# Kernel tuning notes

Measured on AMD Instinct MI355X. Metric: run time of the kernel, lower is better.

## Reference

```python
import jax, jax.numpy as jnp
import numpy as np

B, S, D, H, F = 2, 4096, 768, 12, 3072
DK = D // H
EPS = 1e-5


def _layernorm(x, alpha, gamma):
    # Faithful to the custom Layernormalization: torch.std (unbiased, ddof=1),
    # (x - mean) / (std + eps), scalar alpha/gamma.
    m = jnp.mean(x, axis=-1, keepdims=True)
    s = jnp.std(x, axis=-1, ddof=1, keepdims=True)
    return alpha * ((x - m) / (s + EPS)) + gamma


def setup_inputs() -> dict:
    key = jax.random.key(0)
    ks = jax.random.split(key, 12)
    sc = 0.02
    inp = {
        "x": jax.random.normal(ks[0], (B, S, D), jnp.float32),
        # attention projections, stored as [in, out]
        "wq": jax.random.normal(ks[1], (D, D), jnp.float32) * sc,
        "bq": jnp.zeros((D,), jnp.float32),
        "wk": jax.random.normal(ks[2], (D, D), jnp.float32) * sc,
        "bk": jnp.zeros((D,), jnp.float32),
        "wv": jax.random.normal(ks[3], (D, D), jnp.float32) * sc,
        "bv": jnp.zeros((D,), jnp.float32),
        "wo": jax.random.normal(ks[4], (D, D), jnp.float32) * sc,
        "bo": jnp.zeros((D,), jnp.float32),
        # feedforward
        "w1": jax.random.normal(ks[5], (D, F), jnp.float32) * sc,
        "b1": jnp.zeros((F,), jnp.float32),
        "w2": jax.random.normal(ks[6], (F, D), jnp.float32) * sc,
        "b2": jnp.zeros((D,), jnp.float32),
        # two residual LayerNorms, scalar params (alpha=1, gamma=0 at init)
        "a1": jnp.ones((1,), jnp.float32),
        "g1": jnp.zeros((1,), jnp.float32),
        "a2": jnp.ones((1,), jnp.float32),
        "g2": jnp.zeros((1,), jnp.float32),
    }
    return inp


def reference(x, wq, bq, wk, bk, wv, bv, wo, bo, w1, b1, w2, b2, a1, g1, a2, g2):
    # --- self attention sublayer ---
    q = (x @ wq + bq).reshape(B, S, H, DK).transpose(0, 2, 1, 3)  # [B,H,S,dk]
    k = (x @ wk + bk).reshape(B, S, H, DK).transpose(0, 2, 1, 3)
    v = (x @ wv + bv).reshape(B, S, H, DK).transpose(0, 2, 1, 3)
    scores = jnp.einsum("bhqd,bhkd->bhqk", q, k) / np.sqrt(DK).astype(np.float32)
    attn = jax.nn.softmax(scores, axis=-1)  # dropout is identity (p=0 / eval)
    ctx = jnp.einsum("bhqk,bhkd->bhqd", attn, v)  # [B,H,S,dk]
    ctx = ctx.transpose(0, 2, 1, 3).reshape(B, S, D)
    attn_out = ctx @ wo + bo
    x = _layernorm(x + attn_out, a1, g1)
    # --- feedforward sublayer ---
    ff = jax.nn.relu(x @ w1 + b1) @ w2 + b2
    x = _layernorm(x + ff, a2, g2)
    return x
```

## Files before the change

kernel.cpp:

```cpp
#include <hip/hip_runtime.h>
#include <hip/hip_bf16.h>
#include <cstdint>
#include <cstddef>

typedef unsigned short u16;
typedef __attribute__((ext_vector_type(8))) __bf16 bf16x8;
typedef __attribute__((ext_vector_type(4))) float f32x4;

#define AS1 __attribute__((address_space(1)))
#define AS3 __attribute__((address_space(3)))

__device__ __forceinline__ u16 f2bf(float f) {
    union { float f; uint32_t u; } v; v.f = f;
    uint32_t r = (v.u + 0x7FFFu + ((v.u >> 16) & 1u)) >> 16;
    return (u16)r;
}

__device__ __forceinline__ float bf2f(u16 b) {
    union { uint32_t u; float f; } v; v.u = ((uint32_t)b) << 16;
    return v.f;
}

__device__ __forceinline__ uint32_t pack_bf2(float lo, float hi) {
    __hip_bfloat162 p = __float22bfloat162_rn(float2{lo, hi});
    union { __hip_bfloat162 b; uint32_t u; } v; v.b = p;
    return v.u;
}

__device__ __forceinline__ f32x4 mfma16(bf16x8 a, bf16x8 b, f32x4 c) {
    return __builtin_amdgcn_mfma_f32_16x16x32_bf16(a, b, c, 0, 0, 0);
}

__device__ __forceinline__ void async16(const u16* g, u16* lds_uniform_base) {
    __builtin_amdgcn_global_load_lds((const AS1 void*)g, (AS3 void*)lds_uniform_base, 16, 0, 0);
}

__global__ __launch_bounds__(256)
void k_prep(const float* __restrict__ x, u16* __restrict__ xb,
            const float* __restrict__ wq, const float* __restrict__ wk,
            const float* __restrict__ wv, const float* __restrict__ wo,
            const float* __restrict__ w1, const float* __restrict__ w2,
            u16* __restrict__ wqkvt, u16* __restrict__ wot,
            u16* __restrict__ w1t, u16* __restrict__ w2t)
{
    int bx = blockIdx.x;
    if (bx < 6144) {
        int i = (bx * 256 + threadIdx.x) * 4;
        float4 f = *(const float4*)(x + i);
        xb[i + 0] = f2bf(f.x); xb[i + 1] = f2bf(f.y);
        xb[i + 2] = f2bf(f.z); xb[i + 3] = f2bf(f.w);
        return;
    }
    int t = bx - 6144;
    const float* in; u16* out; int R, C;
    if (t < 2304) {
        int m = t / 576; t -= m * 576;
        R = 768; C = 768;
        in = (m == 0) ? wq : (m == 1) ? wk : (m == 2) ? wv : wo;
        out = (m < 3) ? wqkvt + (size_t)m * 768 * 768 : wot;
    } else if (t < 4608) {
        t -= 2304; in = w1; out = w1t; R = 768; C = 3072;
    } else {
        t -= 4608; in = w2; out = w2t; R = 3072; C = 768;
    }
    int tilesX = C >> 5;
    int c0 = (t % tilesX) * 32, r0 = (t / tilesX) * 32;
    __shared__ float tile[32][33];
    int tx = threadIdx.x & 31, ty = threadIdx.x >> 5;
    #pragma unroll
    for (int i = ty; i < 32; i += 8)
        tile[i][tx] = in[(size_t)(r0 + i) * C + c0 + tx];
    __syncthreads();
    #pragma unroll
    for (int i = ty; i < 32; i += 8)
        out[(size_t)(c0 + i) * R + r0 + tx] = f2bf(tile[tx][i]);
}

template <bool RELU>
__global__ __launch_bounds__(256)
void k_gemm(const u16* __restrict__ A, const u16* __restrict__ Bt,
            const float* __restrict__ bias, u16* __restrict__ Cb,
            int M, int N, int K)
{
    __shared__ __align__(16) u16 lA[128 * 32];
    __shared__ __align__(16) u16 lB[128 * 32];
    const int tid = threadIdx.x;
    const int w = tid >> 6, lane = tid & 63;
    const int quad = lane >> 4, l15 = lane & 15;
    const int m0 = blockIdx.x * 128, n0 = blockIdx.y * 128;
    const int wm = (w >> 1) * 64, wn = (w & 1) * 64;
    const int sw = (quad ^ ((l15 >> 1) & 3)) * 8;

    const f32x4 fz = {0.f, 0.f, 0.f, 0.f};
    f32x4 acc[4][4];
    #pragma unroll
    for (int i = 0; i < 4; ++i)
        #pragma unroll
        for (int j = 0; j < 4; ++j) acc[i][j] = fz;

    for (int k0 = 0; k0 < K; k0 += 32) {
        #pragma unroll
        for (int r = 0; r < 2; ++r) {
            int c = r * 256 + tid;
            int row = c >> 2, ch = (c & 3) ^ ((row >> 1) & 3);
            async16(A + (size_t)(m0 + row) * K + k0 + ch * 8,
                    (u16*)lA + (size_t)(r * 256 + w * 64) * 8);
            async16(Bt + (size_t)(n0 + row) * K + k0 + ch * 8,
                    (u16*)lB + (size_t)(r * 256 + w * 64) * 8);
        }
        __syncthreads();
        bf16x8 af[4], bfr[4];
        #pragma unroll
        for (int i = 0; i < 4; ++i)
            af[i] = *(const bf16x8*)&lA[(wm + i * 16 + l15) * 32 + sw];
        #pragma unroll
        for (int j = 0; j < 4; ++j)
            bfr[j] = *(const bf16x8*)&lB[(wn + j * 16 + l15) * 32 + sw];
        #pragma unroll
        for (int i = 0; i < 4; ++i)
            #pragma unroll
            for (int j = 0; j < 4; ++j)
                acc[i][j] = mfma16(af[i], bfr[j], acc[i][j]);
        __syncthreads();
    }
    #pragma unroll
    for (int j = 0; j < 4; ++j) {
        int col = n0 + wn + j * 16 + l15;
        float bv = bias[col];
        #pragma unroll
        for (int i = 0; i < 4; ++i) {
            int row = m0 + wm + i * 16 + quad * 4;
            #pragma unroll
            for (int r = 0; r < 4; ++r) {
                float t = acc[i][j][r] + bv;
                if (RELU) t = fmaxf(t, 0.f);
                Cb[(size_t)(row + r) * N + col] = f2bf(t);
            }
        }
    }
}

__global__ __launch_bounds__(256)
void k_gemm_part(const u16* __restrict__ A, const u16* __restrict__ Bt,
                 float* __restrict__ C0, float* __restrict__ C1,
                 int M, int N, int K, int Kh)
{
    __shared__ __align__(16) u16 lA[128 * 32];
    __shared__ __align__(16) u16 lB[128 * 32];
    const int tid = threadIdx.x;
    const int w = tid >> 6, lane = tid & 63;
    const int quad = lane >> 4, l15 = lane & 15;
    const int m0 = blockIdx.x * 128, n0 = blockIdx.y * 128;
    const int wm = (w >> 1) * 64, wn = (w & 1) * 64;
    const int sw = (quad ^ ((l15 >> 1) & 3)) * 8;
    const int kbeg = blockIdx.z * Kh, kend = kbeg + Kh;
    float* __restrict__ C = blockIdx.z ? C1 : C0;

    const f32x4 fz = {0.f, 0.f, 0.f, 0.f};
    f32x4 acc[4][4];
    #pragma unroll
    for (int i = 0; i < 4; ++i)
        #pragma unroll
        for (int j = 0; j < 4; ++j) acc[i][j] = fz;

    for (int k0 = kbeg; k0 < kend; k0 += 32) {
        #pragma unroll
        for (int r = 0; r < 2; ++r) {
            int c = r * 256 + tid;
            int row = c >> 2, ch = (c & 3) ^ ((row >> 1) & 3);
            async16(A + (size_t)(m0 + row) * K + k0 + ch * 8,
                    (u16*)lA + (size_t)(r * 256 + w * 64) * 8);
            async16(Bt + (size_t)(n0 + row) * K + k0 + ch * 8,
                    (u16*)lB + (size_t)(r * 256 + w * 64) * 8);
        }
        __syncthreads();
        bf16x8 af[4], bfr[4];
        #pragma unroll
        for (int i = 0; i < 4; ++i)
            af[i] = *(const bf16x8*)&lA[(wm + i * 16 + l15) * 32 + sw];
        #pragma unroll
        for (int j = 0; j < 4; ++j)
            bfr[j] = *(const bf16x8*)&lB[(wn + j * 16 + l15) * 32 + sw];
        #pragma unroll
        for (int i = 0; i < 4; ++i)
            #pragma unroll
            for (int j = 0; j < 4; ++j)
                acc[i][j] = mfma16(af[i], bfr[j], acc[i][j]);
        __syncthreads();
    }
    #pragma unroll
    for (int j = 0; j < 4; ++j) {
        int col = n0 + wn + j * 16 + l15;
        #pragma unroll
        for (int i = 0; i < 4; ++i) {
            int row = m0 + wm + i * 16 + quad * 4;
            #pragma unroll
            for (int r = 0; r < 4; ++r)
                C[(size_t)(row + r) * N + col] = acc[i][j][r];
        }
    }
}

__global__ __launch_bounds__(256)
void k_gemm_qkv(const u16* __restrict__ A, const u16* __restrict__ Bt,
                const float* __restrict__ bq, const float* __restrict__ bk,
                const float* __restrict__ bv,
                u16* __restrict__ qb, u16* __restrict__ kb, u16* __restrict__ vtg,
                int M, int K, float scale_q)
{
    __shared__ __align__(16) u16 qsm[4 * 64 * 72];
    u16* lA = qsm;
    u16* lB = qsm + 4096;
    const int tid = threadIdx.x;
    const int w = tid >> 6, lane = tid & 63;
    const int quad = lane >> 4, l15 = lane & 15;
    const int m0 = blockIdx.x * 128, n0 = blockIdx.y * 128;
    const int wm = (w >> 1) * 64, wn = (w & 1) * 64;
    const int sw = (quad ^ ((l15 >> 1) & 3)) * 8;
    const int sel = blockIdx.y / 6;
    const int cl0 = n0 - sel * 768;

    const f32x4 fz = {0.f, 0.f, 0.f, 0.f};
    f32x4 acc[4][4];
    #pragma unroll
    for (int i = 0; i < 4; ++i)
        #pragma unroll
        for (int j = 0; j < 4; ++j) acc[i][j] = fz;

    for (int k0 = 0; k0 < K; k0 += 32) {
        #pragma unroll
        for (int r = 0; r < 2; ++r) {
            int c = r * 256 + tid;
            int row = c >> 2, ch = (c & 3) ^ ((row >> 1) & 3);
            async16(A + (size_t)(m0 + row) * K + k0 + ch * 8,
                    lA + (size_t)(r * 256 + w * 64) * 8);
            async16(Bt + (size_t)(n0 + row) * K + k0 + ch * 8,
                    lB + (size_t)(r * 256 + w * 64) * 8);
        }
        __syncthreads();
        bf16x8 af[4], bfr[4];
        #pragma unroll
        for (int i = 0; i < 4; ++i)
            af[i] = *(const bf16x8*)&lA[(wm + i * 16 + l15) * 32 + sw];
        #pragma unroll
        for (int j = 0; j < 4; ++j)
            bfr[j] = *(const bf16x8*)&lB[(wn + j * 16 + l15) * 32 + sw];
        #pragma unroll
        for (int i = 0; i < 4; ++i)
            #pragma unroll
            for (int j = 0; j < 4; ++j)
                acc[i][j] = mfma16(af[i], bfr[j], acc[i][j]);
        __syncthreads();
    }
    const float* bias = (sel == 0) ? bq : (sel == 1) ? bk : bv;
    if (sel < 2) {
        u16* out = (sel == 0) ? qb : kb;
        float sc = (sel == 0) ? scale_q : 1.f;
        #pragma unroll
        for (int j = 0; j < 4; ++j) {
            int cl = cl0 + wn + j * 16 + l15;
            float bvv = bias[cl];
            #pragma unroll
            for (int i = 0; i < 4; ++i) {
                int row = m0 + wm + i * 16 + quad * 4;
                #pragma unroll
                for (int r = 0; r < 4; ++r)
                    out[(size_t)(row + r) * 768 + cl] = f2bf((acc[i][j][r] + bvv) * sc);
            }
        }
    } else {
        u16* lT = qsm + w * 4608;
        #pragma unroll
        for (int j = 0; j < 4; ++j) {
            float bvv = bias[cl0 + wn + j * 16 + l15];
            #pragma unroll
            for (int i = 0; i < 4; ++i)
                #pragma unroll
                for (int r = 0; r < 4; ++r)
                    lT[(j * 16 + l15) * 72 + i * 16 + quad * 4 + r]
                        = f2bf(acc[i][j][r] + bvv);
        }
        int gcol = cl0 + wn + lane;
        u16* gdst = vtg + (size_t)gcol * M + m0 + wm;
        #pragma unroll
        for (int kk = 0; kk < 8; ++kk) {
            bf16x8 v = *(const bf16x8*)&lT[lane * 72 + kk * 8];
            *(bf16x8*)(gdst + kk * 8) = v;
        }
    }
}

__global__ __launch_bounds__(256, 3)
void k_attention(const u16* __restrict__ Q, const u16* __restrict__ Kb,
                 const u16* __restrict__ Vt, u16* __restrict__ ctx,
                 int S, int D, int H, int M)
{
    __shared__ __align__(16) u16 sKV[16384];
    __shared__ float sL[2][64];
    const int qt = blockIdx.x, bh = blockIdx.y;
    const int b = bh / H, h = bh % H;
    const int tid = threadIdx.x, w = tid >> 6, lane = tid & 63;
    const int wq = w & 1, wk = w >> 1;
    const int quad = lane >> 4, l15 = lane & 15;
    const int sw = (quad ^ ((l15 >> 1) & 3)) * 8;
    const size_t bS = (size_t)b * S;
    const int q0 = qt * 128 + wq * 64;

    bf16x8 qf[4][2];
    #pragma unroll
    for (int set = 0; set < 4; ++set)
        #pragma unroll
        for (int kc = 0; kc < 2; ++kc)
            qf[set][kc] = *(const bf16x8*)(Q + (bS + q0 + set * 16 + l15) * D
                                           + (size_t)h * 64 + kc * 32 + quad * 8);

    const f32x4 fz = {0.f, 0.f, 0.f, 0.f};
    f32x4 O[4][4], Ol[4];
    #pragma unroll
    for (int s = 0; s < 4; ++s) {
        Ol[s] = fz;
        #pragma unroll
        for (int j = 0; j < 4; ++j) O[s][j] = fz;
    }
    union { u16 s[8]; bf16x8 v; } one8;
    #pragma unroll
    for (int i = 0; i < 8; ++i) one8.s[i] = 0x3F80;

    const u16* kbase = Kb + bS * D + (size_t)h * 64;
    const u16* vbase = Vt + (size_t)h * 64 * M + bS;

    const int rsw = (lane & ~12) | ((lane & 4) << 1) | ((lane & 8) >> 1);
    const u16* gk[2]; const u16* gv[2];
    #pragma unroll
    for (int i = 0; i < 2; ++i) {
        gk[i] = kbase + (size_t)rsw * D + i * 32 + w * 8;
        int c = i * 256 + tid;
        int dk = (c >> 2) & 63, vch = (c & 3) ^ ((dk >> 1) & 3);
        gv[i] = vbase + (size_t)dk * M + i * 32 + vch * 8;
    }
    const int dslot = w * 512;

    #pragma unroll
    for (int i = 0; i < 2; ++i) {
        async16(gk[i], sKV + i * 2048 + dslot);
        async16(gv[i], sKV + 8192 + i * 2048 + dslot);
        gk[i] += (size_t)64 * D;
        gv[i] += 64;
    }

    int ksl[2];
    #pragma unroll
    for (int ks = 0; ks < 2; ++ks) {
        int row64 = wk * 32 + ((l15 >> 2) << 3) + ks * 4 + (l15 & 3);
        int s = (row64 & ~12) | ((row64 & 4) << 1) | ((row64 & 8) >> 1);
        ksl[ks] = quad * 512 + s * 8;
    }

    const int T = S >> 6;
    for (int t = 0; t < T; ++t) {
        __syncthreads();
        if (t + 1 < T) {
            int nb = (t + 1) & 1;
            #pragma unroll
            for (int i = 0; i < 2; ++i) {
                async16(gk[i], sKV + nb * 4096 + i * 2048 + dslot);
                async16(gv[i], sKV + 8192 + nb * 4096 + i * 2048 + dslot);
                gk[i] += (size_t)64 * D;
                gv[i] += 64;
            }
        }
        const u16* lKb = sKV + (t & 1) * 4096;
        const u16* lVb = sKV + 8192 + (t & 1) * 4096;

        bf16x8 ka[2][2], vf[4];
        #pragma unroll
        for (int ks = 0; ks < 2; ++ks)
            #pragma unroll
            for (int kc = 0; kc < 2; ++kc)
                ka[ks][kc] = *(const bf16x8*)&lKb[kc * 2048 + ksl[ks]];
        #pragma unroll
        for (int dj = 0; dj < 4; ++dj)
            vf[dj] = *(const bf16x8*)
                &lVb[wk * 2048 + (dj * 16 + l15) * 32 + sw];

        #pragma unroll
        for (int set = 0; set < 4; ++set) {
            f32x4 sc0 = fz, sc1 = fz;
            __builtin_amdgcn_s_setprio(1);
            sc0 = mfma16(ka[0][0], qf[set][0], sc0);
            sc0 = mfma16(ka[0][1], qf[set][1], sc0);
            sc1 = mfma16(ka[1][0], qf[set][0], sc1);
            sc1 = mfma16(ka[1][1], qf[set][1], sc1);
            __builtin_amdgcn_s_setprio(0);
            float p0[4], p1[4];
            #pragma unroll
            for (int r = 0; r < 4; ++r) {
                p0[r] = __builtin_amdgcn_exp2f(sc0[r]);
                p1[r] = __builtin_amdgcn_exp2f(sc1[r]);
            }
            union { uint32_t u[4]; bf16x8 v; } pa;
            pa.u[0] = pack_bf2(p0[0], p0[1]); pa.u[1] = pack_bf2(p0[2], p0[3]);
            pa.u[2] = pack_bf2(p1[0], p1[1]); pa.u[3] = pack_bf2(p1[2], p1[3]);
            __builtin_amdgcn_s_setprio(1);
            #pragma unroll
            for (int dj = 0; dj < 4; ++dj)
                O[set][dj] = mfma16(pa.v, vf[dj], O[set][dj]);
            Ol[set] = mfma16(pa.v, one8.v, Ol[set]);
            __builtin_amdgcn_s_setprio(0);
        }
    }

    __syncthreads();
    u16* lO = sKV;
    if (wk == 1) {
        #pragma unroll
        for (int set = 0; set < 4; ++set) {
            #pragma unroll
            for (int dj = 0; dj < 4; ++dj)
                #pragma unroll
                for (int r = 0; r < 4; ++r)
                    lO[(wq * 64 + set * 16 + quad * 4 + r) * 66 + dj * 16 + l15]
                        = f2bf(O[set][dj][r]);
            if (l15 == 0) {
                #pragma unroll
                for (int r = 0; r < 4; ++r)
                    sL[wq][set * 16 + quad * 4 + r] = Ol[set][r];
            }
        }
    }
    __syncthreads();
    if (wk == 0) {
        #pragma unroll
        for (int set = 0; set < 4; ++set) {
            float rl[4];
            #pragma unroll
            for (int r = 0; r < 4; ++r)
                rl[r] = 1.f / (Ol[set][r] + sL[wq][set * 16 + quad * 4 + r]);
            #pragma unroll
            for (int dj = 0; dj < 4; ++dj)
                #pragma unroll
                for (int r = 0; r < 4; ++r) {
                    float o = O[set][dj][r]
                        + bf2f(lO[(wq * 64 + set * 16 + quad * 4 + r) * 66 + dj * 16 + l15]);
                    ctx[(bS + q0 + set * 16 + quad * 4 + r) * D
                        + (size_t)h * 64 + dj * 16 + l15] = f2bf(o * rl[r]);
                }
        }
    }
}

__global__ __launch_bounds__(256)
void k_layernorm2(const float* __restrict__ p0, const float* __restrict__ p1,
                  const float* __restrict__ resid, const float* __restrict__ bias,
                  const float* __restrict__ a, const float* __restrict__ g,
                  float* __restrict__ outf, u16* __restrict__ outb, int D)
{
    const int row = blockIdx.x, tid = threadIdx.x;
    const size_t base = (size_t)row * D;
    float v[3];
    float s = 0.f, sq = 0.f;
    #pragma unroll
    for (int i = 0; i < 3; ++i) {
        int c = tid + i * 256;
        float x = p0[base + c] + p1[base + c] + resid[base + c] + bias[c];
        v[i] = x; s += x; sq += x * x;
    }
    #pragma unroll
    for (int off = 32; off >= 1; off >>= 1) {
        s += __shfl_xor(s, off, 64);
        sq += __shfl_xor(sq, off, 64);
    }
    __shared__ float red[8];
    const int w = tid >> 6;
    if ((tid & 63) == 0) { red[w] = s; red[4 + w] = sq; }
    __syncthreads();
    s = red[0] + red[1] + red[2] + red[3];
    sq = red[4] + red[5] + red[6] + red[7];
    float mean = s / D;
    float var = fmaxf((sq - s * mean) / (D - 1), 0.f);
    float denom = sqrtf(var) + 1e-5f;
    float av = a[0], gv = g[0];
    #pragma unroll
    for (int i = 0; i < 3; ++i) {
        float y = av * ((v[i] - mean) / denom) + gv;
        if (outf) outf[base + tid + i * 256] = y;
        if (outb) outb[base + tid + i * 256] = f2bf(y);
    }
}

extern "C" void kernel_launch(void* const* d_in, const int* in_sizes, int n_in,
                              void* d_out, int out_size, void* d_ws, size_t ws_size,
                              hipStream_t stream)
{
    constexpr int B = 2, S = 4096, D = 768, H = 12, F = 3072;
    constexpr int M = B * S;
    const float SCALE_Q = 1.4426950408889634f / 8.0f;
    const float* x  = (const float*)d_in[0];
    const float* wq = (const float*)d_in[1];
    const float* bq = (const float*)d_in[2];
    const float* wk = (const float*)d_in[3];
    const float* bk = (const float*)d_in[4];
    const float* wv = (const float*)d_in[5];
    const float* bv = (const float*)d_in[6];
    const float* wo = (const float*)d_in[7];
    const float* bo = (const float*)d_in[8];
    const float* w1 = (const float*)d_in[9];
    const float* b1 = (const float*)d_in[10];
    const float* w2 = (const float*)d_in[11];
    const float* b2 = (const float*)d_in[12];
    const float* a1 = (const float*)d_in[13];
    const float* g1 = (const float*)d_in[14];
    const float* a2 = (const float*)d_in[15];
    const float* g2 = (const float*)d_in[16];

    char* ws = (char*)d_ws;
    size_t off = 0;
    auto alloc = [&](size_t bytes) {
        void* p = ws + off;
        off = (off + bytes + 255) & ~(size_t)255;
        return p;
    };
    u16*   xb    = (u16*)alloc((size_t)M * D * 2);
    u16*   wqkvt = (u16*)alloc((size_t)3 * D * D * 2);
    u16*   wot   = (u16*)alloc((size_t)D * D * 2);
    u16*   w1t   = (u16*)alloc((size_t)D * F * 2);
    u16*   w2t   = (u16*)alloc((size_t)D * F * 2);
    u16*   qb    = (u16*)alloc((size_t)M * D * 2);
    u16*   kb    = (u16*)alloc((size_t)M * D * 2);
    u16*   vtg   = (u16*)alloc((size_t)M * D * 2);
    u16*   ctxb  = (u16*)alloc((size_t)M * D * 2);
    float* x1f   = (float*)alloc((size_t)M * D * 4);
    u16*   x1b   = (u16*)alloc((size_t)M * D * 2);
    u16*   ff1b  = (u16*)alloc((size_t)M * F * 2);

    float* p0a = (float*)qb;
    float* p1a = (float*)ff1b;
    float* p0b = (float*)qb;
    float* p1b = (float*)vtg;

    k_prep<<<6144 + 6912, 256, 0, stream>>>(x, xb, wq, wk, wv, wo, w1, w2,
                                            wqkvt, wot, w1t, w2t);

    k_gemm_qkv<<<dim3(M / 128, 3 * D / 128), 256, 0, stream>>>(
        xb, wqkvt, bq, bk, bv, qb, kb, vtg, M, D, SCALE_Q);

    k_attention<<<dim3(S / 128, B * H), 256, 0, stream>>>(qb, kb, vtg, ctxb, S, D, H, M);

    k_gemm_part<<<dim3(M / 128, D / 128, 2), 256, 0, stream>>>(
        ctxb, wot, p0a, p1a, M, D, D, D / 2);
    k_layernorm2<<<M, 256, 0, stream>>>(p0a, p1a, x, bo, a1, g1, x1f, x1b, D);

    k_gemm<true><<<dim3(M / 128, F / 128), 256, 0, stream>>>(
        x1b, w1t, b1, ff1b, M, F, D);
    k_gemm_part<<<dim3(M / 128, D / 128, 2), 256, 0, stream>>>(
        ff1b, w2t, p0b, p1b, M, D, F, F / 2);
    k_layernorm2<<<M, 256, 0, stream>>>(p0b, p1b, x1f, b2, a2, g2, (float*)d_out, nullptr, D);

    (void)in_sizes; (void)n_in; (void)out_size; (void)ws_size;
}
```

Baseline: 473.3 us.

## Double-buffer LDS tiles in GEMM kernels and swizzle attention blocks across XCDs

The three GEMM kernels now use two LDS buffers and prefetch the next K-slice with async global-to-LDS loads while the MFMAs run on the current slice. This removes one barrier per iteration and hides load latency behind compute, at the cost of doubling the LDS footprint of the GEMM tiles. The attention kernel remaps its block index so that consecutive logical tiles, which share K/V for the same batch-head, land on the same XCD and can share L2. The swizzle assumes the grid size is a multiple of eight.

After: 451.7 us. 1.05x faster.

```diff
diff --git a/kernel.cpp b/kernel.cpp
--- a/kernel.cpp
+++ b/kernel.cpp
@@ -33,6 +33,11 @@
 
 __device__ __forceinline__ void async16(const u16* g, u16* lds_uniform_base) {
     __builtin_amdgcn_global_load_lds((const AS1 void*)g, (AS3 void*)lds_uniform_base, 16, 0, 0);
+}
+
+__device__ __forceinline__ int xcd_swz(int nwg) {
+    int b = blockIdx.x + gridDim.x * (blockIdx.y + gridDim.y * blockIdx.z);
+    return (b & 7) * (nwg >> 3) + (b >> 3);
 }
 
 __global__ __launch_bounds__(256)
@@ -82,14 +87,24 @@
             const float* __restrict__ bias, u16* __restrict__ Cb,
             int M, int N, int K)
 {
-    __shared__ __align__(16) u16 lA[128 * 32];
-    __shared__ __align__(16) u16 lB[128 * 32];
+    __shared__ __align__(16) u16 lA[2 * 4096];
+    __shared__ __align__(16) u16 lB[2 * 4096];
     const int tid = threadIdx.x;
     const int w = tid >> 6, lane = tid & 63;
     const int quad = lane >> 4, l15 = lane & 15;
     const int m0 = blockIdx.x * 128, n0 = blockIdx.y * 128;
     const int wm = (w >> 1) * 64, wn = (w & 1) * 64;
     const int sw = (quad ^ ((l15 >> 1) & 3)) * 8;
+    const int dst = (w * 64) * 8;
+
+    const u16* pA[2]; const u16* pB[2];
+    #pragma unroll
+    for (int r = 0; r < 2; ++r) {
+        int c = r * 256 + tid;
+        int row = c >> 2, ch = (c & 3) ^ ((row >> 1) & 3);
+        pA[r] = A + (size_t)(m0 + row) * K + ch * 8;
+        pB[r] = Bt + (size_t)(n0 + row) * K + ch * 8;
+    }
 
     const f32x4 fz = {0.f, 0.f, 0.f, 0.f};
     f32x4 acc[4][4];
@@ -98,30 +113,39 @@
         #pragma unroll
         for (int j = 0; j < 4; ++j) acc[i][j] = fz;
 
-    for (int k0 = 0; k0 < K; k0 += 32) {
-        #pragma unroll
-        for (int r = 0; r < 2; ++r) {
-            int c = r * 256 + tid;
-            int row = c >> 2, ch = (c & 3) ^ ((row >> 1) & 3);
-            async16(A + (size_t)(m0 + row) * K + k0 + ch * 8,
-                    (u16*)lA + (size_t)(r * 256 + w * 64) * 8);
-            async16(Bt + (size_t)(n0 + row) * K + k0 + ch * 8,
-                    (u16*)lB + (size_t)(r * 256 + w * 64) * 8);
-        }
+    #pragma unroll
+    for (int r = 0; r < 2; ++r) {
+        async16(pA[r], lA + r * 2048 + dst);
+        async16(pB[r], lB + r * 2048 + dst);
+        pA[r] += 32; pB[r] += 32;
+    }
+
+    const int nIt = K >> 5;
+    for (int it = 0; it < nIt; ++it) {
         __syncthreads();
+        if (it + 1 < nIt) {
+            int nb = (it + 1) & 1;
+            #pragma unroll
+            for (int r = 0; r < 2; ++r) {
+                async16(pA[r], lA + nb * 4096 + r * 2048 + dst);
+                async16(pB[r], lB + nb * 4096 + r * 2048 + dst);
+                pA[r] += 32; pB[r] += 32;
+            }
+        }
+        const u16* bA = lA + (it & 1) * 4096;
+        const u16* bB = lB + (it & 1) * 4096;
         bf16x8 af[4], bfr[4];
         #pragma unroll
         for (int i = 0; i < 4; ++i)
-            af[i] = *(const bf16x8*)&lA[(wm + i * 16 + l15) * 32 + sw];
+            af[i] = *(const bf16x8*)&bA[(wm + i * 16 + l15) * 32 + sw];
         #pragma unroll
         for (int j = 0; j < 4; ++j)
-            bfr[j] = *(const bf16x8*)&lB[(wn + j * 16 + l15) * 32 + sw];
+            bfr[j] = *(const bf16x8*)&bB[(wn + j * 16 + l15) * 32 + sw];
         #pragma unroll
         for (int i = 0; i < 4; ++i)
             #pragma unroll
             for (int j = 0; j < 4; ++j)
                 acc[i][j] = mfma16(af[i], bfr[j], acc[i][j]);
-        __syncthreads();
     }
     #pragma unroll
     for (int j = 0; j < 4; ++j) {
@@ -145,16 +169,26 @@
                  float* __restrict__ C0, float* __restrict__ C1,
                  int M, int N, int K, int Kh)
 {
-    __shared__ __align__(16) u16 lA[128 * 32];
-    __shared__ __align__(16) u16 lB[128 * 32];
+    __shared__ __align__(16) u16 lA[2 * 4096];
+    __shared__ __align__(16) u16 lB[2 * 4096];
     const int tid = threadIdx.x;
     const int w = tid >> 6, lane = tid & 63;
     const int quad = lane >> 4, l15 = lane & 15;
     const int m0 = blockIdx.x * 128, n0 = blockIdx.y * 128;
     const int wm = (w >> 1) * 64, wn = (w & 1) * 64;
     const int sw = (quad ^ ((l15 >> 1) & 3)) * 8;
-    const int kbeg = blockIdx.z * Kh, kend = kbeg + Kh;
+    const int kbeg = blockIdx.z * Kh;
     float* __restrict__ C = blockIdx.z ? C1 : C0;
+    const int dst = (w * 64) * 8;
+
+    const u16* pA[2]; const u16* pB[2];
+    #pragma unroll
+    for (int r = 0; r < 2; ++r) {
+        int c = r * 256 + tid;
+        int row = c >> 2, ch = (c & 3) ^ ((row >> 1) & 3);
+        pA[r] = A + (size_t)(m0 + row) * K + kbeg + ch * 8;
+        pB[r] = Bt + (size_t)(n0 + row) * K + kbeg + ch * 8;
+    }
 
     const f32x4 fz = {0.f, 0.f, 0.f, 0.f};
     f32x4 acc[4][4];
@@ -163,30 +197,39 @@
         #pragma unroll
         for (int j = 0; j < 4; ++j) acc[i][j] = fz;
 
-    for (int k0 = kbeg; k0 < kend; k0 += 32) {
-        #pragma unroll
-        for (int r = 0; r < 2; ++r) {
-            int c = r * 256 + tid;
-            int row = c >> 2, ch = (c & 3) ^ ((row >> 1) & 3);
-            async16(A + (size_t)(m0 + row) * K + k0 + ch * 8,
-                    (u16*)lA + (size_t)(r * 256 + w * 64) * 8);
-            async16(Bt + (size_t)(n0 + row) * K + k0 + ch * 8,
-                    (u16*)lB + (size_t)(r * 256 + w * 64) * 8);
-        }
+    #pragma unroll
+    for (int r = 0; r < 2; ++r) {
+        async16(pA[r], lA + r * 2048 + dst);
+        async16(pB[r], lB + r * 2048 + dst);
+        pA[r] += 32; pB[r] += 32;
+    }
+
+    const int nIt = Kh >> 5;
+    for (int it = 0; it < nIt; ++it) {
         __syncthreads();
+        if (it + 1 < nIt) {
+            int nb = (it + 1) & 1;
+            #pragma unroll
+            for (int r = 0; r < 2; ++r) {
+                async16(pA[r], lA + nb * 4096 + r * 2048 + dst);
+                async16(pB[r], lB + nb * 4096 + r * 2048 + dst);
+                pA[r] += 32; pB[r] += 32;
+            }
+        }
+        const u16* bA = lA + (it & 1) * 4096;
+        const u16* bB = lB + (it & 1) * 4096;
         bf16x8 af[4], bfr[4];
         #pragma unroll
         for (int i = 0; i < 4; ++i)
-            af[i] = *(const bf16x8*)&lA[(wm + i * 16 + l15) * 32 + sw];
+            af[i] = *(const bf16x8*)&bA[(wm + i * 16 + l15) * 32 + sw];
         #pragma unroll
         for (int j = 0; j < 4; ++j)
-            bfr[j] = *(const bf16x8*)&lB[(wn + j * 16 + l15) * 32 + sw];
+            bfr[j] = *(const bf16x8*)&bB[(wn + j * 16 + l15) * 32 + sw];
         #pragma unroll
         for (int i = 0; i < 4; ++i)
             #pragma unroll
             for (int j = 0; j < 4; ++j)
                 acc[i][j] = mfma16(af[i], bfr[j], acc[i][j]);
-        __syncthreads();
     }
     #pragma unroll
     for (int j = 0; j < 4; ++j) {
@@ -210,7 +253,7 @@
 {
     __shared__ __align__(16) u16 qsm[4 * 64 * 72];
     u16* lA = qsm;
-    u16* lB = qsm + 4096;
+    u16* lB = qsm + 8192;
     const int tid = threadIdx.x;
     const int w = tid >> 6, lane = tid & 63;
     const int quad = lane >> 4, l15 = lane & 15;
@@ -219,6 +262,16 @@
     const int sw = (quad ^ ((l15 >> 1) & 3)) * 8;
     const int sel = blockIdx.y / 6;
     const int cl0 = n0 - sel * 768;
+    const int dst = (w * 64) * 8;
+
+    const u16* pA[2]; const u16* pB[2];
+    #pragma unroll
+    for (int r = 0; r < 2; ++r) {
+        int c = r * 256 + tid;
+        int row = c >> 2, ch = (c & 3) ^ ((row >> 1) & 3);
+        pA[r] = A + (size_t)(m0 + row) * K + ch * 8;
+        pB[r] = Bt + (size_t)(n0 + row) * K + ch * 8;
+    }
 
     const f32x4 fz = {0.f, 0.f, 0.f, 0.f};
     f32x4 acc[4][4];
@@ -227,31 +280,41 @@
         #pragma unroll
         for (int j = 0; j < 4; ++j) acc[i][j] = fz;
 
-    for (int k0 = 0; k0 < K; k0 += 32) {
-        #pragma unroll
-        for (int r = 0; r < 2; ++r) {
-            int c = r * 256 + tid;
-            int row = c >> 2, ch = (c & 3) ^ ((row >> 1) & 3);
-            async16(A + (size_t)(m0 + row) * K + k0 + ch * 8,
-                    lA + (size_t)(r * 256 + w * 64) * 8);
-            async16(Bt + (size_t)(n0 + row) * K + k0 + ch * 8,
-                    lB + (size_t)(r * 256 + w * 64) * 8);
-        }
+    #pragma unroll
+    for (int r = 0; r < 2; ++r) {
+        async16(pA[r], lA + r * 2048 + dst);
+        async16(pB[r], lB + r * 2048 + dst);
+        pA[r] += 32; pB[r] += 32;
+    }
+
+    const int nIt = K >> 5;
+    for (int it = 0; it < nIt; ++it) {
         __syncthreads();
+        if (it + 1 < nIt) {
+            int nb = (it + 1) & 1;
+            #pragma unroll
+            for (int r = 0; r < 2; ++r) {
+                async16(pA[r], lA + nb * 4096 + r * 2048 + dst);
+                async16(pB[r], lB + nb * 4096 + r * 2048 + dst);
+                pA[r] += 32; pB[r] += 32;
+            }
+        }
+        const u16* bA = lA + (it & 1) * 4096;
+        const u16* bB = lB + (it & 1) * 4096;
         bf16x8 af[4], bfr[4];
         #pragma unroll
         for (int i = 0; i < 4; ++i)
-            af[i] = *(const bf16x8*)&lA[(wm + i * 16 + l15) * 32 + sw];
+            af[i] = *(const bf16x8*)&bA[(wm + i * 16 + l15) * 32 + sw];
         #pragma unroll
         for (int j = 0; j < 4; ++j)
-            bfr[j] = *(const bf16x8*)&lB[(wn + j * 16 + l15) * 32 + sw];
+            bfr[j] = *(const bf16x8*)&bB[(wn + j * 16 + l15) * 32 + sw];
         #pragma unroll
         for (int i = 0; i < 4; ++i)
             #pragma unroll
             for (int j = 0; j < 4; ++j)
                 acc[i][j] = mfma16(af[i], bfr[j], acc[i][j]);
-        __syncthreads();
-    }
+    }
+    __syncthreads();
     const float* bias = (sel == 0) ? bq : (sel == 1) ? bk : bv;
     if (sel < 2) {
         u16* out = (sel == 0) ? qb : kb;
@@ -297,7 +360,8 @@
 {
     __shared__ __align__(16) u16 sKV[16384];
     __shared__ float sL[2][64];
-    const int qt = blockIdx.x, bh = blockIdx.y;
+    const int o = xcd_swz(gridDim.x * gridDim.y);
+    const int qt = o % gridDim.x, bh = o / gridDim.x;
     const int b = bh / H, h = bh % H;
     const int tid = threadIdx.x, w = tid >> 6, lane = tid & 63;
     const int wq = w & 1, wk = w >> 1;
```
